# Performance work log

Measured on AMD Instinct MI355X. Metric: run time of the kernel, lower is better.

The kernel has to match this reference:

```python
import jax, jax.numpy as jnp
import numpy as np

NEG = -10000.0

def _wn(W, g):
    # weight_norm with dim=None: single scalar g scaling W / ||W||_F
    return g * W / jnp.linalg.norm(W)

def setup_inputs() -> dict:
    key = jax.random.key(0)
    ks = jax.random.split(key, 10)
    B, N, H, P = 128, 4096, 128, 128
    v = jax.random.normal(ks[0], (B, N, H), jnp.float32)
    q = jax.random.normal(ks[1], (B, H), jnp.float32)
    mask = jnp.ones((B, N), jnp.float32)
    # params (out_dim, in_dim) like torch Linear
    Wv = jax.random.normal(ks[2], (P, H), jnp.float32) / np.sqrt(H)
    bv = jnp.zeros((P,), jnp.float32)
    gv = jnp.float32(jnp.linalg.norm(Wv))
    Wq = jax.random.normal(ks[3], (P, H), jnp.float32) / np.sqrt(H)
    bq = jnp.zeros((P,), jnp.float32)
    gq = jnp.float32(jnp.linalg.norm(Wq))
    Wa = jax.random.normal(ks[4], (1, P), jnp.float32) / np.sqrt(P)
    ba = jnp.zeros((1,), jnp.float32)
    ga = jnp.float32(jnp.linalg.norm(Wa))
    return {"v": v, "q": q, "mask": mask, "Wv": Wv, "bv": bv, "gv": gv,
            "Wq": Wq, "bq": bq, "gq": gq, "Wa": Wa, "ba": ba, "ga": ga}

def reference(v, q, mask, Wv, bv, gv, Wq, bq, gq, Wa, ba, ga):
    # FCNet projections (dropout is identity at inference; FCNet applies no relu)
    v_proj = jnp.einsum('bnh,ph->bnp', v, _wn(Wv, gv)) + bv        # [B,N,P]
    q_proj = (q @ _wn(Wq, gq).T + bq)[:, None, :]                   # [B,1,P]
    h = jax.nn.relu(v_proj + q_proj)                                # [B,N,P]
    logits = jnp.einsum('bnp,p->bn', h, _wn(Wa, ga)[0]) + ba[0]     # [B,N]
    logits = logits + (1.0 - mask) * NEG
    w = jax.nn.softmax(logits, axis=-1)                             # [B,N]
    w_att = w[:, :, None]                                           # [B,N,1]
    att = jnp.sum(v * w_att, axis=1)                                # [B,H]
    return att, w_att
```

## Files before the change

### kernel.cpp

```cpp
#include <hip/hip_runtime.h>

typedef _Float16 half8_t __attribute__((ext_vector_type(8)));
typedef float f32x4 __attribute__((ext_vector_type(4)));

#define B_ 128
#define N_ 4096
#define H_ 128
#define P_ 128
#define CCH 8
#define ROWS_PER_CHUNK (N_ / CCH)
#define TILES (ROWS_PER_CHUNK / 64)

#define OFF_LOGITS 24832
#define OFF_PART   549120

__global__ __launch_bounds__(256) void k1_main(
    const float* __restrict__ v, const float* __restrict__ mask,
    const float* __restrict__ ba,
    const float* __restrict__ q, const float* __restrict__ Wq,
    const float* __restrict__ bq, const float* __restrict__ bv,
    const float* __restrict__ Wv, const float* __restrict__ gv,
    const float* __restrict__ gq, const float* __restrict__ Wa,
    const float* __restrict__ ga,
    float* __restrict__ ws)
{
    const int c = blockIdx.x;
    const int b = blockIdx.y;
    const int tid = threadIdx.x;
    const int lane = tid & 63;
    const int w = tid >> 6;

    __shared__ __align__(16) _Float16 Bl[16384];
    __shared__ float qpcs[P_];
    __shared__ float was[P_];
    __shared__ float smask[ROWS_PER_CHUNK];
    __shared__ float obuf[4][P_];
    __shared__ float mbuf[4], lbuf[4];
    __shared__ float red3[4][3];

    float sv2 = 0.f, sq2 = 0.f, sa2 = 0.f;

#pragma unroll
    for (int g = 0; g < 8; ++g) {
        const int idx = w * 8 + g;
        const int kk = idx >> 3, pt = idx & 7;
        const int p = pt * 16 + (lane & 15);
        const int h = kk * 32 + (lane >> 4) * 8;
        const float4* src = (const float4*)(Wv + (size_t)p * H_ + h);
        float4 f0 = src[0], f1 = src[1];
        sv2 += f0.x * f0.x + f0.y * f0.y + f0.z * f0.z + f0.w * f0.w
             + f1.x * f1.x + f1.y * f1.y + f1.z * f1.z + f1.w * f1.w;
        half8_t a;
        a[0] = (_Float16)f0.x; a[1] = (_Float16)f0.y;
        a[2] = (_Float16)f0.z; a[3] = (_Float16)f0.w;
        a[4] = (_Float16)f1.x; a[5] = (_Float16)f1.y;
        a[6] = (_Float16)f1.z; a[7] = (_Float16)f1.w;
        *(half8_t*)&Bl[(((kk * 8 + pt) * 64) + lane) * 8] = a;
    }

    {
        const int p  = tid >> 1;
        const int hh = tid & 1;
        const float4* qr = (const float4*)(q + (size_t)b * H_) + hh * 16;
        const float4* wr = (const float4*)(Wq + (size_t)p * H_) + hh * 16;
        float dot = 0.f;
#pragma unroll
        for (int i = 0; i < 16; ++i) {
            float4 a = qr[i], c4 = wr[i];
            dot += a.x * c4.x + a.y * c4.y + a.z * c4.z + a.w * c4.w;
            sq2 += c4.x * c4.x + c4.y * c4.y + c4.z * c4.z + c4.w * c4.w;
        }
        dot += __shfl_xor(dot, 1, 64);
        if (hh == 0) qpcs[p] = dot;
    }

    float wa_z = 0.f;
    if (tid < P_) { wa_z = Wa[tid]; sa2 = wa_z * wa_z; }

#pragma unroll
    for (int i = 0; i < ROWS_PER_CHUNK / 256; ++i)
        smask[tid + i * 256] = mask[(size_t)b * N_ + c * ROWS_PER_CHUNK + tid + i * 256];

#pragma unroll
    for (int m = 1; m <= 32; m <<= 1) {
        sv2 += __shfl_xor(sv2, m, 64);
        sq2 += __shfl_xor(sq2, m, 64);
        sa2 += __shfl_xor(sa2, m, 64);
    }
    if (lane == 0) { red3[w][0] = sv2; red3[w][1] = sq2; red3[w][2] = sa2; }
    __syncthreads();
    const float nv = red3[0][0] + red3[1][0] + red3[2][0] + red3[3][0];
    const float nq = red3[0][1] + red3[1][1] + red3[2][1] + red3[3][1];
    const float na = red3[0][2] + red3[1][2] + red3[2][2] + red3[3][2];
    const float rnv = sqrtf(nv);
    const float sv = gv[0] / rnv;
    const float inv_sv = rnv / gv[0];
    const float sq = gq[0] / sqrtf(nq);
    const float sa = ga[0] / sqrtf(na);

    if (tid < P_) {
        qpcs[tid] = (qpcs[tid] * sq + bq[tid] + bv[tid]) * inv_sv;
        was[tid]  = wa_z * (sa * sv);
    }
    const float ba0 = ba[0];
    __syncthreads();

    const int rloc = lane & 15;
    const int grp  = lane >> 4;
    const int colb = grp * 8;

    float m_w = -1e30f, l_w = 0.f;
    float o32[32];
#pragma unroll
    for (int j = 0; j < 32; ++j) o32[j] = 0.f;

    for (int it = 0; it < TILES; ++it) {
        const int r0 = it * 64 + w * 16;
        const int n0w = c * ROWS_PER_CHUNK + r0;

        const float* vrow = v + ((size_t)b * N_ + n0w + rloc) * H_;
        half8_t af[4];
#pragma unroll
        for (int kk = 0; kk < 4; ++kk) {
            const float4* p4 = (const float4*)(vrow + kk * 32 + colb);
            float4 f0 = p4[0], f1 = p4[1];
            half8_t a;
            a[0] = (_Float16)f0.x; a[1] = (_Float16)f0.y;
            a[2] = (_Float16)f0.z; a[3] = (_Float16)f0.w;
            a[4] = (_Float16)f1.x; a[5] = (_Float16)f1.y;
            a[6] = (_Float16)f1.z; a[7] = (_Float16)f1.w;
            af[kk] = a;
        }

        float lp[4];
        lp[0] = lp[1] = lp[2] = lp[3] = 0.f;
#pragma unroll
        for (int pt = 0; pt < 8; ++pt) {
            const int p = pt * 16 + rloc;
            const float qv = qpcs[p];
            f32x4 acc = {qv, qv, qv, qv};
#pragma unroll
            for (int kk = 0; kk < 4; ++kk) {
                half8_t bf = *(const half8_t*)&Bl[(((kk * 8 + pt) * 64) + lane) * 8];
                acc = __builtin_amdgcn_mfma_f32_16x16x32_f16(af[kk], bf, acc, 0, 0, 0);
            }
            const float wv = was[p];
#pragma unroll
            for (int r = 0; r < 4; ++r)
                lp[r] += fmaxf(acc[r], 0.f) * wv;
        }
#pragma unroll
        for (int m = 1; m <= 8; m <<= 1) {
#pragma unroll
            for (int r = 0; r < 4; ++r) lp[r] += __shfl_xor(lp[r], m, 64);
        }
#pragma unroll
        for (int r = 0; r < 4; ++r) {
            const float mk = smask[r0 + grp * 4 + r];
            lp[r] += ba0 + (1.0f - mk) * (-10000.0f);
        }

        const int srcl = (rloc >> 2) << 4;
        float t0 = __shfl(lp[0], srcl, 64);
        float t1 = __shfl(lp[1], srcl, 64);
        float t2 = __shfl(lp[2], srcl, 64);
        float t3 = __shfl(lp[3], srcl, 64);
        float a01 = (rloc & 1) ? t1 : t0;
        float a23 = (rloc & 1) ? t3 : t2;
        float lg_me = (rloc & 2) ? a23 : a01;

        if (lane < 16) ws[OFF_LOGITS + (size_t)b * N_ + n0w + lane] = lg_me;

        float mt = fmaxf(fmaxf(lp[0], lp[1]), fmaxf(lp[2], lp[3]));
        mt = fmaxf(mt, __shfl_xor(mt, 16, 64));
        mt = fmaxf(mt, __shfl_xor(mt, 32, 64));

        const float mn = fmaxf(m_w, mt);
        const float alpha = __expf(m_w - mn);
        const float wme = __expf(lg_me - mn);
        float s = wme;
#pragma unroll
        for (int m = 1; m <= 8; m <<= 1) s += __shfl_xor(s, m, 64);
        l_w = l_w * alpha + s;
        m_w = mn;

        if (alpha != 1.0f) {
#pragma unroll
            for (int j = 0; j < 32; ++j) o32[j] *= alpha;
        }
#pragma unroll
        for (int kk = 0; kk < 4; ++kk) {
#pragma unroll
            for (int j = 0; j < 8; ++j)
                o32[kk * 8 + j] += wme * (float)af[kk][j];
        }
    }

#pragma unroll
    for (int m = 1; m <= 8; m <<= 1) {
#pragma unroll
        for (int j = 0; j < 32; ++j) o32[j] += __shfl_xor(o32[j], m, 64);
    }
    {
        const int j0 = rloc * 2;
#pragma unroll
        for (int u = 0; u < 2; ++u) {
            const int j = j0 + u;
            obuf[w][(j >> 3) * 32 + colb + (j & 7)] = o32[j];
        }
        if (lane == 0) { mbuf[w] = m_w; lbuf[w] = l_w; }
    }
    __syncthreads();

    float* part = ws + OFF_PART + ((size_t)b * CCH + c) * 132;
    if (tid < P_) {
        const float mb = fmaxf(fmaxf(mbuf[0], mbuf[1]), fmaxf(mbuf[2], mbuf[3]));
        float lb = 0.f, oh = 0.f;
#pragma unroll
        for (int ww = 0; ww < 4; ++ww) {
            const float e = __expf(mbuf[ww] - mb);
            lb += e * lbuf[ww];
            oh += e * obuf[ww][tid];
        }
        part[2 + tid] = oh;
        if (tid == 0) { part[0] = mb; part[1] = lb; }
    }
}

__global__ __launch_bounds__(256) void k2_final(
    const float* __restrict__ ws, float* __restrict__ out)
{
    const int c4 = blockIdx.x;
    const int b  = blockIdx.y;
    const int tid = threadIdx.x;
    const float* part = ws + OFF_PART + (size_t)b * CCH * 132;

    float m = -1e30f;
#pragma unroll
    for (int cc = 0; cc < CCH; ++cc) m = fmaxf(m, part[cc * 132]);
    float l = 0.f;
#pragma unroll
    for (int cc = 0; cc < CCH; ++cc)
        l += __expf(part[cc * 132] - m) * part[cc * 132 + 1];
    const float il = 1.0f / l;

    if (c4 == 0 && tid < P_) {
        float a = 0.f;
#pragma unroll
        for (int cc = 0; cc < CCH; ++cc)
            a += __expf(part[cc * 132] - m) * part[cc * 132 + 2 + tid];
        out[(size_t)b * H_ + tid] = a * il;
    }

    const float4* lg4 = (const float4*)(ws + OFF_LOGITS + (size_t)b * N_ + c4 * 1024);
    float4* w4 = (float4*)(out + B_ * H_ + (size_t)b * N_ + c4 * 1024);
    float4 g = lg4[tid];
    float4 r;
    r.x = __expf(g.x - m) * il;
    r.y = __expf(g.y - m) * il;
    r.z = __expf(g.z - m) * il;
    r.w = __expf(g.w - m) * il;
    w4[tid] = r;
}

extern "C" void kernel_launch(void* const* d_in, const int* in_sizes, int n_in,
                              void* d_out, int out_size, void* d_ws, size_t ws_size,
                              hipStream_t stream) {
    const float* v    = (const float*)d_in[0];
    const float* q    = (const float*)d_in[1];
    const float* mask = (const float*)d_in[2];
    const float* Wv   = (const float*)d_in[3];
    const float* bv   = (const float*)d_in[4];
    const float* gv   = (const float*)d_in[5];
    const float* Wq   = (const float*)d_in[6];
    const float* bq   = (const float*)d_in[7];
    const float* gq   = (const float*)d_in[8];
    const float* Wa   = (const float*)d_in[9];
    const float* ba   = (const float*)d_in[10];
    const float* ga   = (const float*)d_in[11];
    float* out = (float*)d_out;
    float* ws  = (float*)d_ws;

    k1_main<<<dim3(CCH, B_), 256, 0, stream>>>(v, mask, ba, q, Wq, bq, bv,
                                               Wv, gv, gq, Wa, ga, ws);
    k2_final<<<dim3(4, B_), 256, 0, stream>>>(ws, out);
}
```

Measured before the change: 405.9 us.

## Move weight-norm and q-projection prep into a separate kernel

```diff
diff --git a/kernel.cpp b/kernel.cpp
--- a/kernel.cpp
+++ b/kernel.cpp
@@ -11,59 +11,38 @@
 #define ROWS_PER_CHUNK (N_ / CCH)
 #define TILES (ROWS_PER_CHUNK / 64)
 
+#define OFF_WA     16
+#define OFF_QPC    256
+#define OFF_BPACK  16640
 #define OFF_LOGITS 24832
 #define OFF_PART   549120
 
-__global__ __launch_bounds__(256) void k1_main(
-    const float* __restrict__ v, const float* __restrict__ mask,
-    const float* __restrict__ ba,
-    const float* __restrict__ q, const float* __restrict__ Wq,
+__global__ __launch_bounds__(256) void k0_prep(
+    const float* __restrict__ q,  const float* __restrict__ Wq,
     const float* __restrict__ bq, const float* __restrict__ bv,
     const float* __restrict__ Wv, const float* __restrict__ gv,
     const float* __restrict__ gq, const float* __restrict__ Wa,
-    const float* __restrict__ ga,
-    float* __restrict__ ws)
+    const float* __restrict__ ga, float* __restrict__ ws)
 {
-    const int c = blockIdx.x;
-    const int b = blockIdx.y;
+    const int b = blockIdx.x;
     const int tid = threadIdx.x;
     const int lane = tid & 63;
     const int w = tid >> 6;
-
-    __shared__ __align__(16) _Float16 Bl[16384];
-    __shared__ float qpcs[P_];
-    __shared__ float was[P_];
-    __shared__ float smask[ROWS_PER_CHUNK];
-    __shared__ float obuf[4][P_];
-    __shared__ float mbuf[4], lbuf[4];
     __shared__ float red3[4][3];
 
     float sv2 = 0.f, sq2 = 0.f, sa2 = 0.f;
-
-#pragma unroll
-    for (int g = 0; g < 8; ++g) {
-        const int idx = w * 8 + g;
-        const int kk = idx >> 3, pt = idx & 7;
-        const int p = pt * 16 + (lane & 15);
-        const int h = kk * 32 + (lane >> 4) * 8;
-        const float4* src = (const float4*)(Wv + (size_t)p * H_ + h);
-        float4 f0 = src[0], f1 = src[1];
-        sv2 += f0.x * f0.x + f0.y * f0.y + f0.z * f0.z + f0.w * f0.w
-             + f1.x * f1.x + f1.y * f1.y + f1.z * f1.z + f1.w * f1.w;
-        half8_t a;
-        a[0] = (_Float16)f0.x; a[1] = (_Float16)f0.y;
-        a[2] = (_Float16)f0.z; a[3] = (_Float16)f0.w;
-        a[4] = (_Float16)f1.x; a[5] = (_Float16)f1.y;
-        a[6] = (_Float16)f1.z; a[7] = (_Float16)f1.w;
-        *(half8_t*)&Bl[(((kk * 8 + pt) * 64) + lane) * 8] = a;
-    }
-
+    const float4* Wv4 = (const float4*)Wv;
+#pragma unroll
+    for (int i = 0; i < 16; ++i) {
+        float4 a = Wv4[tid + i * 256];
+        sv2 += a.x * a.x + a.y * a.y + a.z * a.z + a.w * a.w;
+    }
+
+    const int p = tid >> 1, hh = tid & 1;
+    float dot = 0.f;
     {
-        const int p  = tid >> 1;
-        const int hh = tid & 1;
         const float4* qr = (const float4*)(q + (size_t)b * H_) + hh * 16;
         const float4* wr = (const float4*)(Wq + (size_t)p * H_) + hh * 16;
-        float dot = 0.f;
 #pragma unroll
         for (int i = 0; i < 16; ++i) {
             float4 a = qr[i], c4 = wr[i];
@@ -71,15 +50,10 @@
             sq2 += c4.x * c4.x + c4.y * c4.y + c4.z * c4.z + c4.w * c4.w;
         }
         dot += __shfl_xor(dot, 1, 64);
-        if (hh == 0) qpcs[p] = dot;
     }
 
     float wa_z = 0.f;
     if (tid < P_) { wa_z = Wa[tid]; sa2 = wa_z * wa_z; }
-
-#pragma unroll
-    for (int i = 0; i < ROWS_PER_CHUNK / 256; ++i)
-        smask[tid + i * 256] = mask[(size_t)b * N_ + c * ROWS_PER_CHUNK + tid + i * 256];
 
 #pragma unroll
     for (int m = 1; m <= 32; m <<= 1) {
@@ -98,11 +72,59 @@
     const float sq = gq[0] / sqrtf(nq);
     const float sa = ga[0] / sqrtf(na);
 
-    if (tid < P_) {
-        qpcs[tid] = (qpcs[tid] * sq + bq[tid] + bv[tid]) * inv_sv;
-        was[tid]  = wa_z * (sa * sv);
-    }
-    const float ba0 = ba[0];
+    if (hh == 0)
+        ws[OFF_QPC + (size_t)b * P_ + p] = (dot * sq + bq[p] + bv[p]) * inv_sv;
+
+    if (b == 0) {
+        if (tid < P_) ws[OFF_WA + tid] = wa_z * (sa * sv);
+        _Float16* bp = (_Float16*)(ws + OFF_BPACK);
+#pragma unroll
+        for (int k = 0; k < 64; ++k) {
+            int s  = tid + k * 256;
+            int j  = s & 7;
+            int L  = (s >> 3) & 63;
+            int pt = (s >> 9) & 7;
+            int kk = s >> 12;
+            int pp = pt * 16 + (L & 15);
+            int h  = kk * 32 + (L >> 4) * 8 + j;
+            bp[s] = (_Float16)Wv[pp * H_ + h];
+        }
+    }
+}
+
+__global__ __launch_bounds__(256) void k1_main(
+    const float* __restrict__ v, const float* __restrict__ mask,
+    const float* __restrict__ ba, float* __restrict__ ws)
+{
+    const int c = blockIdx.x;
+    const int b = blockIdx.y;
+    const int tid = threadIdx.x;
+    const int lane = tid & 63;
+    const int w = tid >> 6;
+
+    __shared__ __align__(16) _Float16 Bl[16384];
+    __shared__ float qpcs[P_];
+    __shared__ float was[P_];
+    __shared__ float smask[ROWS_PER_CHUNK];
+    __shared__ float obuf[4][P_];
+    __shared__ float mbuf[4], lbuf[4];
+
+    {
+        const float ba0 = ba[0];
+        const uint4* src = (const uint4*)(ws + OFF_BPACK);
+        uint4* dst = (uint4*)Bl;
+#pragma unroll
+        for (int i = 0; i < 8; ++i) dst[tid + i * 256] = src[tid + i * 256];
+        if (tid < P_) {
+            qpcs[tid] = ws[OFF_QPC + (size_t)b * P_ + tid];
+            was[tid]  = ws[OFF_WA + tid];
+        }
+#pragma unroll
+        for (int i = 0; i < ROWS_PER_CHUNK / 256; ++i) {
+            const float mk = mask[(size_t)b * N_ + c * ROWS_PER_CHUNK + tid + i * 256];
+            smask[tid + i * 256] = ba0 + (1.0f - mk) * (-10000.0f);
+        }
+    }
     __syncthreads();
 
     const int rloc = lane & 15;
@@ -155,10 +177,17 @@
             for (int r = 0; r < 4; ++r) lp[r] += __shfl_xor(lp[r], m, 64);
         }
 #pragma unroll
-        for (int r = 0; r < 4; ++r) {
-            const float mk = smask[r0 + grp * 4 + r];
-            lp[r] += ba0 + (1.0f - mk) * (-10000.0f);
-        }
+        for (int r = 0; r < 4; ++r) lp[r] += smask[r0 + grp * 4 + r];
+
+        float mt = fmaxf(fmaxf(lp[0], lp[1]), fmaxf(lp[2], lp[3]));
+        mt = fmaxf(mt, __shfl_xor(mt, 16, 64));
+        mt = fmaxf(mt, __shfl_xor(mt, 32, 64));
+        const float mn = fmaxf(m_w, mt);
+
+        float sg = __expf(lp[0] - mn) + __expf(lp[1] - mn)
+                 + __expf(lp[2] - mn) + __expf(lp[3] - mn);
+        sg += __shfl_xor(sg, 16, 64);
+        sg += __shfl_xor(sg, 32, 64);
 
         const int srcl = (rloc >> 2) << 4;
         float t0 = __shfl(lp[0], srcl, 64);
@@ -171,17 +200,9 @@
 
         if (lane < 16) ws[OFF_LOGITS + (size_t)b * N_ + n0w + lane] = lg_me;
 
-        float mt = fmaxf(fmaxf(lp[0], lp[1]), fmaxf(lp[2], lp[3]));
-        mt = fmaxf(mt, __shfl_xor(mt, 16, 64));
-        mt = fmaxf(mt, __shfl_xor(mt, 32, 64));
-
-        const float mn = fmaxf(m_w, mt);
         const float alpha = __expf(m_w - mn);
         const float wme = __expf(lg_me - mn);
-        float s = wme;
-#pragma unroll
-        for (int m = 1; m <= 8; m <<= 1) s += __shfl_xor(s, m, 64);
-        l_w = l_w * alpha + s;
+        l_w = l_w * alpha + sg;
         m_w = mn;
 
         if (alpha != 1.0f) {
@@ -281,7 +302,7 @@
     float* out = (float*)d_out;
     float* ws  = (float*)d_ws;
 
-    k1_main<<<dim3(CCH, B_), 256, 0, stream>>>(v, mask, ba, q, Wq, bq, bv,
-                                               Wv, gv, gq, Wa, ga, ws);
+    k0_prep<<<B_, 256, 0, stream>>>(q, Wq, bq, bv, Wv, gv, gq, Wa, ga, ws);
+    k1_main<<<dim3(CCH, B_), 256, 0, stream>>>(v, mask, ba, ws);
     k2_final<<<dim3(4, B_), 256, 0, stream>>>(ws, out);
 }
```

New measurement: 412.7 us. About the same (+1.7%).
